# Kernel optimization log

Measured on AMD Instinct MI355X. Metric: run time of the kernel, lower is better.

Reference implementation:

```python
import jax, jax.numpy as jnp
import numpy as np

T, B, H = 2048, 64, 256   # time, batch, hidden/input/memory size
A = 256                   # attention_size
IN = H + H                # cell input size = input_size + memory_size = 512
NEG = -1e12


def setup_inputs() -> dict:
    key = jax.random.key(0)
    ks = jax.random.split(key, 12)
    s = lambda k, shape, fan: jax.random.normal(k, shape, jnp.float32) / np.sqrt(fan)
    inp = {
        "input": jax.random.normal(ks[0], (B, H), jnp.float32),
        "memory": jax.random.normal(ks[1], (T, B, H), jnp.float32),
        "memory_mask": jax.random.bernoulli(ks[2], 0.9, (T, B)),
        "state": jax.random.normal(ks[3], (B, H), jnp.float32),
        # attention MLP: Linear(input+state+memory -> A, no bias), Tanh, Linear(A -> 1, no bias)
        "W_a1": s(ks[4], (H + H + H, A), H * 3),
        "w_a2": s(ks[5], (A,), A),
        # gate: Linear(IN -> IN, no bias) + sigmoid
        "W_gate": s(ks[6], (IN, IN), IN),
        # GRUCell params (torch layout: [3H, in], gates order r,z,n)
        "W_ih": s(ks[7], (3 * H, IN), IN),
        "W_hh": s(ks[8], (3 * H, H), H),
        "b_ih": jnp.zeros((3 * H,), jnp.float32),
        "b_hh": jnp.zeros((3 * H,), jnp.float32),
    }
    return inp


def reference(input, memory, memory_mask, state, W_a1, w_a2, W_gate, W_ih, W_hh, b_ih, b_hh):
    # --- additive attention: tanh(W1 @ [input, state, memory]) @ w2 ---
    # split W_a1 by the concat layout [input | state | memory]
    qs = jnp.concatenate([input, state], axis=-1) @ W_a1[: 2 * H]      # [B, A]
    mp = jnp.einsum("tbh,ha->tba", memory, W_a1[2 * H :])               # [T, B, A]
    logits = jnp.tanh(qs[None] + mp) @ w_a2                              # [T, B]
    logits = jnp.where(memory_mask, logits, NEG)
    scores = jax.nn.softmax(logits, axis=0)                              # [T, B]
    attn_vec = jnp.einsum("tb,tbh->bh", scores, memory)                  # [B, H]

    # --- gate ---
    new_input = jnp.concatenate([input, attn_vec], axis=-1)              # [B, 2H]
    gated = new_input * jax.nn.sigmoid(new_input @ W_gate)

    # --- GRU cell (torch semantics, gates r, z, n) ---
    gi = gated @ W_ih.T + b_ih                                           # [B, 3H]
    gh = state @ W_hh.T + b_hh                                           # [B, 3H]
    i_r, i_z, i_n = jnp.split(gi, 3, axis=-1)
    h_r, h_z, h_n = jnp.split(gh, 3, axis=-1)
    r = jax.nn.sigmoid(i_r + h_r)
    z = jax.nn.sigmoid(i_z + h_z)
    n = jnp.tanh(i_n + r * h_n)
    return (1.0 - z) * n + z * state                                     # [B, H]
```

## Files before the change

kernel.cpp:

```cpp
#include <hip/hip_runtime.h>
#include <hip/hip_bf16.h>

#define B_DIM 64
#define H_DIM 256
#define NCHG 4
#define CHUNKS 8
#define TCH 64
#define NEG_INF -1e12f

typedef __attribute__((ext_vector_type(8))) short short8;
typedef __attribute__((ext_vector_type(4))) float f32x4;

typedef const __attribute__((address_space(1))) void gas_void;
typedef __attribute__((address_space(3))) void las_void;

__device__ __forceinline__ unsigned short bfbits(float f) {
    __hip_bfloat16 h = __float2bfloat16(f);
    unsigned short u;
    __builtin_memcpy(&u, &h, 2);
    return u;
}
__device__ __forceinline__ float fast_tanh(float x) {
    float e = __expf(2.0f * x);
    return 1.0f - 2.0f / (e + 1.0f);
}
__device__ __forceinline__ float fast_sigmoid(float x) {
    return 1.0f / (1.0f + __expf(-x));
}

__global__ void prep_qs_kernel(const float* __restrict__ W_a1,
                               const float* __restrict__ input,
                               const float* __restrict__ state,
                               unsigned short* __restrict__ WmT,
                               float* __restrict__ qs) {
    __shared__ float cat[512];
    int bid = blockIdx.x, tid = threadIdx.x;
    if (bid < 256) {
        WmT[tid * 256 + bid] = bfbits(W_a1[(512 + bid) * 256 + tid]);
    } else {
        int b = bid - 256;
        cat[tid] = input[b * 256 + tid];
        cat[256 + tid] = state[b * 256 + tid];
        __syncthreads();
        int a = tid;
        float s0 = 0.f, s1 = 0.f, s2 = 0.f, s3 = 0.f;
        #pragma unroll 4
        for (int k = 0; k < 512; k += 4) {
            s0 += cat[k]     * W_a1[(k)     * 256 + a];
            s1 += cat[k + 1] * W_a1[(k + 1) * 256 + a];
            s2 += cat[k + 2] * W_a1[(k + 2) * 256 + a];
            s3 += cat[k + 3] * W_a1[(k + 3) * 256 + a];
        }
        qs[b * 256 + a] = (s0 + s1) + (s2 + s3);
    }
}

__global__ __launch_bounds__(512, 1) void attn_kernel(
    const float* __restrict__ memory, const int* __restrict__ mask,
    const unsigned short* __restrict__ WmT,
    const float* __restrict__ qs, const float* __restrict__ w_a2,
    float* __restrict__ part_m, float* __restrict__ part_l,
    float* __restrict__ part_acc)
{
    extern __shared__ char smem[];
    float* slabF = (float*)smem;
    unsigned short* slabB = (unsigned short*)(smem + 65536);
    float* lpart = (float*)(smem + 65536 + 32768);
    float* pbuf  = lpart + 512;

    int b = blockIdx.x, g = blockIdx.y;
    int tid = threadIdx.x;
    int lane = tid & 63, w = tid >> 6;
    int lr = lane & 15, lh = lane >> 4;
    int tbase = g * (CHUNKS * TCH);
    const char* mbase = (const char*)(memory + (size_t)tbase * (B_DIM * H_DIM) + b * H_DIM);

    int wa0 = w * 32;
    float qv[2][4], wv[2][4];
    #pragma unroll
    for (int mf = 0; mf < 2; ++mf)
        #pragma unroll
        for (int r = 0; r < 4; ++r) {
            int a = wa0 + mf * 16 + lh * 4 + r;
            qv[mf][r] = qs[b * 256 + a];
            wv[mf][r] = w_a2[a];
        }

    auto stage = [&](int s) {
        #pragma unroll
        for (int i = 0; i < 8; ++i) {
            int row = w * 8 + i;
            const char* gp = mbase + (size_t)(s * TCH + row) * (B_DIM * H_DIM * 4)
                           + ((lane * 16) ^ ((row & 7) << 4));
            __builtin_amdgcn_global_load_lds((gas_void*)gp,
                                             (las_void*)&slabF[row * 256], 16, 0, 0);
        }
    };

    stage(0);
    __syncthreads();

    float a8[8] = {0.f, 0.f, 0.f, 0.f, 0.f, 0.f, 0.f, 0.f};
    float M = -3.4e38f, L = 0.f;
    int oct = tid & 31, slice = tid >> 5;
    int h0 = oct * 8;
    int crow = tid & 63, cseg = tid >> 6;
    int csw = (crow & 7) << 4;

    for (int s = 0; s < CHUNKS; ++s) {
        #pragma unroll
        for (int j = 0; j < 4; ++j) {
            int k0 = cseg * 32 + j * 8;
            float4 v0 = *(const float4*)((const char*)(slabF + crow * 256) + (((k0 * 4))      ^ csw));
            float4 v1 = *(const float4*)((const char*)(slabF + crow * 256) + (((k0 * 4) + 16) ^ csw));
            ushort4 o0, o1;
            o0.x = bfbits(v0.x); o0.y = bfbits(v0.y); o0.z = bfbits(v0.z); o0.w = bfbits(v0.w);
            o1.x = bfbits(v1.x); o1.y = bfbits(v1.y); o1.z = bfbits(v1.z); o1.w = bfbits(v1.w);
            *(ushort4*)((char*)(slabB + crow * 256) + ((k0 * 2) ^ csw))     = o0;
            *(ushort4*)((char*)(slabB + crow * 256) + (((k0 * 2) + 8) ^ ((csw & 8) ? csw : csw))) = o1;
        }
        __syncthreads();

        if (s < CHUNKS - 1) stage(s + 1);

        f32x4 acc[2][4];
        #pragma unroll
        for (int mf = 0; mf < 2; ++mf)
            #pragma unroll
            for (int nf = 0; nf < 4; ++nf)
                acc[mf][nf] = (f32x4){0.f, 0.f, 0.f, 0.f};
        #pragma unroll
        for (int kk = 0; kk < 8; ++kk) {
            short8 afr[2];
            #pragma unroll
            for (int mf = 0; mf < 2; ++mf) {
                int a = wa0 + mf * 16 + lr;
                afr[mf] = *(const short8*)(WmT + a * 256 + kk * 32 + lh * 8);
            }
            int kbyte = kk * 64 + lh * 16;
            #pragma unroll
            for (int nf = 0; nf < 4; ++nf) {
                int t = nf * 16 + lr;
                int sw = kbyte ^ ((t & 7) << 4);
                short8 bfr = *(const short8*)((const char*)(slabB + t * 256) + sw);
                #pragma unroll
                for (int mf = 0; mf < 2; ++mf)
                    acc[mf][nf] = __builtin_amdgcn_mfma_f32_16x16x32_bf16(afr[mf], bfr, acc[mf][nf], 0, 0, 0);
            }
        }

        #pragma unroll
        for (int nf = 0; nf < 4; ++nf) {
            float sv = 0.f;
            #pragma unroll
            for (int mf = 0; mf < 2; ++mf)
                #pragma unroll
                for (int r = 0; r < 4; ++r)
                    sv += wv[mf][r] * fast_tanh(qv[mf][r] + acc[mf][nf][r]);
            sv += __shfl_xor(sv, 16);
            sv += __shfl_xor(sv, 32);
            if (lh == 0) lpart[w * 64 + nf * 16 + lr] = sv;
        }
        __syncthreads();

        float lg = 0.f;
        #pragma unroll
        for (int ww = 0; ww < 8; ++ww) lg += lpart[ww * 64 + lane];
        int tglob = tbase + s * TCH + lane;
        lg = mask[tglob * B_DIM + b] ? lg : NEG_INF;
        if (w == 0) pbuf[lane] = lg;
        float mx = lg;
        #pragma unroll
        for (int d = 1; d < 64; d <<= 1) mx = fmaxf(mx, __shfl_xor(mx, d));
        float ex = __expf(lg - mx);
        float sm = ex;
        #pragma unroll
        for (int d = 1; d < 64; d <<= 1) sm += __shfl_xor(sm, d);

        float newM = fmaxf(M, mx);
        float fo = __expf(M - newM);
        L = L * fo + sm * __expf(mx - newM);
        M = newM;
        #pragma unroll
        for (int j = 0; j < 8; ++j) a8[j] *= fo;
        __syncthreads();

        #pragma unroll
        for (int tt = 0; tt < 4; ++tt) {
            int tl = slice * 4 + tt;
            float pt = __expf(pbuf[tl] - M);
            int swb = (h0 * 2) ^ ((tl & 7) << 4);
            uint4 u = *(const uint4*)((const char*)(slabB + tl * 256) + swb);
            a8[0] += pt * __uint_as_float(u.x << 16);
            a8[1] += pt * __uint_as_float(u.x & 0xFFFF0000u);
            a8[2] += pt * __uint_as_float(u.y << 16);
            a8[3] += pt * __uint_as_float(u.y & 0xFFFF0000u);
            a8[4] += pt * __uint_as_float(u.z << 16);
            a8[5] += pt * __uint_as_float(u.z & 0xFFFF0000u);
            a8[6] += pt * __uint_as_float(u.w << 16);
            a8[7] += pt * __uint_as_float(u.w & 0xFFFF0000u);
        }
        __syncthreads();
    }

    float* acc2 = (float*)slabF;
    *(float4*)(&acc2[slice * 256 + h0])     = (float4){a8[0], a8[1], a8[2], a8[3]};
    *(float4*)(&acc2[slice * 256 + h0 + 4]) = (float4){a8[4], a8[5], a8[6], a8[7]};
    __syncthreads();
    int pidx = g * B_DIM + b;
    if (tid < 256) {
        float ssum = 0.f;
        #pragma unroll
        for (int sl = 0; sl < 16; ++sl) ssum += acc2[sl * 256 + tid];
        part_acc[(size_t)pidx * 256 + tid] = ssum;
    }
    if (tid == 0) { part_m[pidx] = M; part_l[pidx] = L; }
}

__global__ void mergegate_kernel(const float* __restrict__ part_m,
                                 const float* __restrict__ part_l,
                                 const float* __restrict__ part_acc,
                                 const float* __restrict__ input,
                                 const float* __restrict__ W_gate,
                                 float* __restrict__ gated) {
    __shared__ float ni[512];
    int b = blockIdx.x, tid = threadIdx.x;
    if (tid >= 256) {
        int k = tid - 256;
        ni[k] = input[b * 256 + k];
    } else {
        int h = tid;
        float M = -3.4e38f;
        #pragma unroll
        for (int c = 0; c < NCHG; ++c) M = fmaxf(M, part_m[c * 64 + b]);
        float L = 0.f, s = 0.f;
        #pragma unroll
        for (int c = 0; c < NCHG; ++c) {
            float sc = __expf(part_m[c * 64 + b] - M);
            L += part_l[c * 64 + b] * sc;
            s += sc * part_acc[(size_t)(c * 64 + b) * 256 + h];
        }
        ni[256 + h] = s / L;
    }
    __syncthreads();
    int j = tid;
    float s0 = 0.f, s1 = 0.f, s2 = 0.f, s3 = 0.f;
    #pragma unroll 4
    for (int k = 0; k < 512; k += 4) {
        s0 += ni[k]     * W_gate[(k)     * 512 + j];
        s1 += ni[k + 1] * W_gate[(k + 1) * 512 + j];
        s2 += ni[k + 2] * W_gate[(k + 2) * 512 + j];
        s3 += ni[k + 3] * W_gate[(k + 3) * 512 + j];
    }
    float s = (s0 + s1) + (s2 + s3);
    gated[b * 512 + j] = ni[j] * fast_sigmoid(s);
}

__global__ __launch_bounds__(768) void gru_kernel(
    const float* __restrict__ gated, const float* __restrict__ state,
    const float* __restrict__ W_ih, const float* __restrict__ W_hh,
    const float* __restrict__ b_ih, const float* __restrict__ b_hh,
    float* __restrict__ out) {
    __shared__ float ld_g[4][512];
    __shared__ float ld_s[4][256];
    __shared__ float xi[3][16][4];
    __shared__ float xh[3][16][4];
    int ht = blockIdx.x & 15, bt = blockIdx.x >> 4;
    int tid = threadIdx.x;
    #pragma unroll
    for (int i = 0; i < 3; ++i) {
        int idx = i * 768 + tid;
        if (idx < 2048) ld_g[idx >> 9][idx & 511] = gated[(bt * 4 + (idx >> 9)) * 512 + (idx & 511)];
    }
    #pragma unroll
    for (int i = 0; i < 2; ++i) {
        int idx = i * 768 + tid;
        if (idx < 1024) ld_s[idx >> 8][idx & 255] = state[(bt * 4 + (idx >> 8)) * 256 + (idx & 255)];
    }

    int gid = tid >> 4, lk = tid & 15;
    int gate = gid >> 4, hl = gid & 15;
    int j = gate * 256 + ht * 16 + hl;

    float4 wi[8], wh[4];
    #pragma unroll
    for (int it = 0; it < 8; ++it)
        wi[it] = *(const float4*)(W_ih + (size_t)j * 512 + it * 64 + lk * 4);
    #pragma unroll
    for (int it = 0; it < 4; ++it)
        wh[it] = *(const float4*)(W_hh + (size_t)j * 256 + it * 64 + lk * 4);
    float bi = b_ih[j], bh = b_hh[j];
    __syncthreads();

    #pragma unroll
    for (int bb = 0; bb < 4; ++bb) {
        float g0 = 0.f, g1 = 0.f;
        #pragma unroll
        for (int it = 0; it < 8; ++it) {
            float4 gv = *(const float4*)(&ld_g[bb][it * 64 + lk * 4]);
            g0 += wi[it].x * gv.x + wi[it].z * gv.z;
            g1 += wi[it].y * gv.y + wi[it].w * gv.w;
        }
        float h0 = 0.f, h1 = 0.f;
        #pragma unroll
        for (int it = 0; it < 4; ++it) {
            float4 sv = *(const float4*)(&ld_s[bb][it * 64 + lk * 4]);
            h0 += wh[it].x * sv.x + wh[it].z * sv.z;
            h1 += wh[it].y * sv.y + wh[it].w * sv.w;
        }
        float gi_ = g0 + g1, gh_ = h0 + h1;
        #pragma unroll
        for (int m = 1; m < 16; m <<= 1) {
            gi_ += __shfl_xor(gi_, m);
            gh_ += __shfl_xor(gh_, m);
        }
        if (lk == 0) { xi[gate][hl][bb] = gi_ + bi; xh[gate][hl][bb] = gh_ + bh; }
    }
    __syncthreads();
    if (tid < 64) {
        int bb = tid >> 4, hl2 = tid & 15;
        float ir = xi[0][hl2][bb], hr = xh[0][hl2][bb];
        float iz = xi[1][hl2][bb], hz = xh[1][hl2][bb];
        float in_ = xi[2][hl2][bb], hn = xh[2][hl2][bb];
        float r = fast_sigmoid(ir + hr);
        float z = fast_sigmoid(iz + hz);
        float n = fast_tanh(in_ + r * hn);
        out[(bt * 4 + bb) * 256 + ht * 16 + hl2] =
            (1.f - z) * n + z * ld_s[bb][ht * 16 + hl2];
    }
}

extern "C" void kernel_launch(void* const* d_in, const int* in_sizes, int n_in,
                              void* d_out, int out_size, void* d_ws, size_t ws_size,
                              hipStream_t stream) {
    const float* input  = (const float*)d_in[0];
    const float* memory = (const float*)d_in[1];
    const int*   mask   = (const int*)d_in[2];
    const float* state  = (const float*)d_in[3];
    const float* W_a1   = (const float*)d_in[4];
    const float* w_a2   = (const float*)d_in[5];
    const float* W_gate = (const float*)d_in[6];
    const float* W_ih   = (const float*)d_in[7];
    const float* W_hh   = (const float*)d_in[8];
    const float* b_ih   = (const float*)d_in[9];
    const float* b_hh   = (const float*)d_in[10];
    float* out = (float*)d_out;

    char* ws = (char*)d_ws;
    unsigned short* WmT = (unsigned short*)(ws + 0);
    float* qs       = (float*)(ws + 131072);
    float* gated    = (float*)(ws + 196608);
    float* part_m   = (float*)(ws + 327680);
    float* part_l   = (float*)(ws + 331776);
    float* part_acc = (float*)(ws + 335872);

    prep_qs_kernel<<<320, 256, 0, stream>>>(W_a1, input, state, WmT, qs);

    (void)hipFuncSetAttribute((const void*)attn_kernel,
                              hipFuncAttributeMaxDynamicSharedMemorySize, 101376);
    attn_kernel<<<dim3(B_DIM, NCHG), 512, 101376, stream>>>(
        memory, mask, WmT, qs, w_a2, part_m, part_l, part_acc);

    mergegate_kernel<<<64, 512, 0, stream>>>(part_m, part_l, part_acc, input, W_gate, gated);
    gru_kernel<<<256, 768, 0, stream>>>(gated, state, W_ih, W_hh, b_ih, b_hh, out);
}
```

Measured before the change: 93.54 us.

## Register-prefetch memory into double-buffered bf16 LDS slabs and keep Wm fragments in registers

Replaces the global_load_lds fp32 staging plus separate LDS conversion pass with register prefetch of the next chunk, issued before the MFMA work and converted to bf16 into a second LDS slab afterwards. The WmT A-fragments are loaded once into registers instead of being reloaded every chunk. The mask is preloaded into LDS, and probabilities are broadcast by shuffle instead of through an LDS buffer, which removes one barrier per chunk. LDS use drops from about 99KB to 68KB and launch bounds allow 2 blocks per CU, at the cost of more registers for the prefetch and A-fragment arrays.

```diff
diff --git a/kernel.cpp b/kernel.cpp
--- a/kernel.cpp
+++ b/kernel.cpp
@@ -10,9 +10,6 @@
 
 typedef __attribute__((ext_vector_type(8))) short short8;
 typedef __attribute__((ext_vector_type(4))) float f32x4;
-
-typedef const __attribute__((address_space(1))) void gas_void;
-typedef __attribute__((address_space(3))) void las_void;
 
 __device__ __forceinline__ unsigned short bfbits(float f) {
     __hip_bfloat16 h = __float2bfloat16(f);
@@ -55,7 +52,7 @@
     }
 }
 
-__global__ __launch_bounds__(512, 1) void attn_kernel(
+__global__ __launch_bounds__(512, 2) void attn_kernel(
     const float* __restrict__ memory, const int* __restrict__ mask,
     const unsigned short* __restrict__ WmT,
     const float* __restrict__ qs, const float* __restrict__ w_a2,
@@ -63,19 +60,31 @@
     float* __restrict__ part_acc)
 {
     extern __shared__ char smem[];
-    float* slabF = (float*)smem;
-    unsigned short* slabB = (unsigned short*)(smem + 65536);
-    float* lpart = (float*)(smem + 65536 + 32768);
-    float* pbuf  = lpart + 512;
+    unsigned short* slab0 = (unsigned short*)smem;
+    unsigned short* slab1 = (unsigned short*)(smem + 32768);
+    float* lpart = (float*)(smem + 65536);
+    int*   maskL = (int*)(smem + 65536 + 2048);
 
     int b = blockIdx.x, g = blockIdx.y;
     int tid = threadIdx.x;
     int lane = tid & 63, w = tid >> 6;
     int lr = lane & 15, lh = lane >> 4;
     int tbase = g * (CHUNKS * TCH);
-    const char* mbase = (const char*)(memory + (size_t)tbase * (B_DIM * H_DIM) + b * H_DIM);
+    const float* mbase = memory + (size_t)tbase * (B_DIM * H_DIM) + b * H_DIM;
+
+    float4 ld[8];
+    #pragma unroll
+    for (int i = 0; i < 8; ++i)
+        ld[i] = *((const float4*)(mbase + (size_t)(i * 8 + w) * (B_DIM * H_DIM)) + lane);
 
     int wa0 = w * 32;
+    short8 areg[8][2];
+    #pragma unroll
+    for (int kk = 0; kk < 8; ++kk)
+        #pragma unroll
+        for (int mf = 0; mf < 2; ++mf)
+            areg[kk][mf] = *(const short8*)(WmT + (wa0 + mf * 16 + lr) * 256 + kk * 32 + lh * 8);
+
     float qv[2][4], wv[2][4];
     #pragma unroll
     for (int mf = 0; mf < 2; ++mf)
@@ -86,42 +95,34 @@
             wv[mf][r] = w_a2[a];
         }
 
-    auto stage = [&](int s) {
-        #pragma unroll
-        for (int i = 0; i < 8; ++i) {
-            int row = w * 8 + i;
-            const char* gp = mbase + (size_t)(s * TCH + row) * (B_DIM * H_DIM * 4)
-                           + ((lane * 16) ^ ((row & 7) << 4));
-            __builtin_amdgcn_global_load_lds((gas_void*)gp,
-                                             (las_void*)&slabF[row * 256], 16, 0, 0);
-        }
-    };
-
-    stage(0);
+    maskL[tid] = mask[(tbase + tid) * B_DIM + b];
+
+    int wby = (lane * 8) ^ (w << 4);
+    #pragma unroll
+    for (int i = 0; i < 8; ++i) {
+        ushort4 o;
+        o.x = bfbits(ld[i].x); o.y = bfbits(ld[i].y);
+        o.z = bfbits(ld[i].z); o.w = bfbits(ld[i].w);
+        *(ushort4*)((char*)slab0 + (i * 8 + w) * 512 + wby) = o;
+    }
     __syncthreads();
 
     float a8[8] = {0.f, 0.f, 0.f, 0.f, 0.f, 0.f, 0.f, 0.f};
     float M = -3.4e38f, L = 0.f;
-    int oct = tid & 31, slice = tid >> 5;
-    int h0 = oct * 8;
-    int crow = tid & 63, cseg = tid >> 6;
-    int csw = (crow & 7) << 4;
+    int slice4 = ((lane >> 5) + 2 * w) * 4;
+    int hpvb = (lane & 31) * 16;
 
     for (int s = 0; s < CHUNKS; ++s) {
-        #pragma unroll
-        for (int j = 0; j < 4; ++j) {
-            int k0 = cseg * 32 + j * 8;
-            float4 v0 = *(const float4*)((const char*)(slabF + crow * 256) + (((k0 * 4))      ^ csw));
-            float4 v1 = *(const float4*)((const char*)(slabF + crow * 256) + (((k0 * 4) + 16) ^ csw));
-            ushort4 o0, o1;
-            o0.x = bfbits(v0.x); o0.y = bfbits(v0.y); o0.z = bfbits(v0.z); o0.w = bfbits(v0.w);
-            o1.x = bfbits(v1.x); o1.y = bfbits(v1.y); o1.z = bfbits(v1.z); o1.w = bfbits(v1.w);
-            *(ushort4*)((char*)(slabB + crow * 256) + ((k0 * 2) ^ csw))     = o0;
-            *(ushort4*)((char*)(slabB + crow * 256) + (((k0 * 2) + 8) ^ ((csw & 8) ? csw : csw))) = o1;
-        }
-        __syncthreads();
-
-        if (s < CHUNKS - 1) stage(s + 1);
+        const char* cur = (const char*)((s & 1) ? slab1 : slab0);
+        char* nxt = (char*)((s & 1) ? slab0 : slab1);
+
+        if (s < CHUNKS - 1) {
+            #pragma unroll
+            for (int i = 0; i < 8; ++i) {
+                int row = (s + 1) * TCH + i * 8 + w;
+                ld[i] = *((const float4*)(mbase + (size_t)row * (B_DIM * H_DIM)) + lane);
+            }
+        }
 
         f32x4 acc[2][4];
         #pragma unroll
@@ -131,21 +132,14 @@
                 acc[mf][nf] = (f32x4){0.f, 0.f, 0.f, 0.f};
         #pragma unroll
         for (int kk = 0; kk < 8; ++kk) {
-            short8 afr[2];
-            #pragma unroll
-            for (int mf = 0; mf < 2; ++mf) {
-                int a = wa0 + mf * 16 + lr;
-                afr[mf] = *(const short8*)(WmT + a * 256 + kk * 32 + lh * 8);
-            }
             int kbyte = kk * 64 + lh * 16;
             #pragma unroll
             for (int nf = 0; nf < 4; ++nf) {
                 int t = nf * 16 + lr;
                 int sw = kbyte ^ ((t & 7) << 4);
-                short8 bfr = *(const short8*)((const char*)(slabB + t * 256) + sw);
-                #pragma unroll
-                for (int mf = 0; mf < 2; ++mf)
-                    acc[mf][nf] = __builtin_amdgcn_mfma_f32_16x16x32_bf16(afr[mf], bfr, acc[mf][nf], 0, 0, 0);
+                short8 bfr = *(const short8*)(cur + t * 512 + sw);
+                acc[0][nf] = __builtin_amdgcn_mfma_f32_16x16x32_bf16(areg[kk][0], bfr, acc[0][nf], 0, 0, 0);
+                acc[1][nf] = __builtin_amdgcn_mfma_f32_16x16x32_bf16(areg[kk][1], bfr, acc[1][nf], 0, 0, 0);
             }
         }
 
@@ -166,9 +160,7 @@
         float lg = 0.f;
         #pragma unroll
         for (int ww = 0; ww < 8; ++ww) lg += lpart[ww * 64 + lane];
-        int tglob = tbase + s * TCH + lane;
-        lg = mask[tglob * B_DIM + b] ? lg : NEG_INF;
-        if (w == 0) pbuf[lane] = lg;
+        lg = maskL[s * 64 + lane] ? lg : NEG_INF;
         float mx = lg;
         #pragma unroll
         for (int d = 1; d < 64; d <<= 1) mx = fmaxf(mx, __shfl_xor(mx, d));
@@ -183,14 +175,14 @@
         M = newM;
         #pragma unroll
         for (int j = 0; j < 8; ++j) a8[j] *= fo;
-        __syncthreads();
+        float pself = __expf(lg - M);
 
         #pragma unroll
         for (int tt = 0; tt < 4; ++tt) {
-            int tl = slice * 4 + tt;
-            float pt = __expf(pbuf[tl] - M);
-            int swb = (h0 * 2) ^ ((tl & 7) << 4);
-            uint4 u = *(const uint4*)((const char*)(slabB + tl * 256) + swb);
+            int tl = slice4 + tt;
+            float pt = __shfl(pself, tl);
+            int swb = hpvb ^ ((tl & 7) << 4);
+            uint4 u = *(const uint4*)(cur + tl * 512 + swb);
             a8[0] += pt * __uint_as_float(u.x << 16);
             a8[1] += pt * __uint_as_float(u.x & 0xFFFF0000u);
             a8[2] += pt * __uint_as_float(u.y << 16);
@@ -200,10 +192,21 @@
             a8[6] += pt * __uint_as_float(u.w << 16);
             a8[7] += pt * __uint_as_float(u.w & 0xFFFF0000u);
         }
+
+        if (s < CHUNKS - 1) {
+            #pragma unroll
+            for (int i = 0; i < 8; ++i) {
+                ushort4 o;
+                o.x = bfbits(ld[i].x); o.y = bfbits(ld[i].y);
+                o.z = bfbits(ld[i].z); o.w = bfbits(ld[i].w);
+                *(ushort4*)(nxt + (i * 8 + w) * 512 + wby) = o;
+            }
+        }
         __syncthreads();
     }
 
-    float* acc2 = (float*)slabF;
+    float* acc2 = (float*)smem;
+    int oct = lane & 31, slice = 2 * w + (lane >> 5), h0 = oct * 8;
     *(float4*)(&acc2[slice * 256 + h0])     = (float4){a8[0], a8[1], a8[2], a8[3]};
     *(float4*)(&acc2[slice * 256 + h0 + 4]) = (float4){a8[4], a8[5], a8[6], a8[7]};
     __syncthreads();
@@ -357,8 +360,8 @@
     prep_qs_kernel<<<320, 256, 0, stream>>>(W_a1, input, state, WmT, qs);
 
     (void)hipFuncSetAttribute((const void*)attn_kernel,
-                              hipFuncAttributeMaxDynamicSharedMemorySize, 101376);
-    attn_kernel<<<dim3(B_DIM, NCHG), 512, 101376, stream>>>(
+                              hipFuncAttributeMaxDynamicSharedMemorySize, 69632);
+    attn_kernel<<<dim3(B_DIM, NCHG), 512, 69632, stream>>>(
         memory, mask, WmT, qs, w_a2, part_m, part_l, part_acc);
 
     mergegate_kernel<<<64, 512, 0, stream>>>(part_m, part_l, part_acc, input, W_gate, gated);
```

Measured after the change: 85.29 us. 1.1x faster.
